# Kernel tuning notes

Hardware: AMD Instinct MI355X
Metric: run time of the kernel (lower is better)

The kernel has to match this reference:

```python
import jax, jax.numpy as jnp
import numpy as np

B, N, C = 2, 2048, 768
H = 16
D = C // H  # head_dim = 48
SCALE = 1.0 / float(np.sqrt(D))


def setup_inputs() -> dict:
    key = jax.random.key(0)
    ks = jax.random.split(key, 5)
    x = jax.random.normal(ks[0], (B, N, C), dtype=jnp.float32)
    # torch nn.Linear weights are [out, in]; apply as x @ W.T
    qkv_w = jax.random.normal(ks[1], (3 * C, C), dtype=jnp.float32) * 0.02
    qkv_b = jax.random.normal(ks[2], (3 * C,), dtype=jnp.float32) * 0.02
    proj_w = jax.random.normal(ks[3], (C, C), dtype=jnp.float32) * 0.02
    proj_b = jax.random.normal(ks[4], (C,), dtype=jnp.float32) * 0.02
    return {"x": x, "qkv_w": qkv_w, "qkv_b": qkv_b, "proj_w": proj_w, "proj_b": proj_b}


def reference(x, qkv_w, qkv_b, proj_w, proj_b):
    # qkv: (B, N, 3C) -> (3, B, H, N, D)
    qkv = x @ qkv_w.T + qkv_b
    qkv = qkv.reshape(B, N, 3, H, D).transpose(2, 0, 3, 1, 4)
    q, k, v = qkv[0], qkv[1], qkv[2]
    # manual attention: full (B, H, N, N) score matrix, as in the original
    attn = jnp.einsum('bhqd,bhkd->bhqk', q, k) * SCALE
    attn = jax.nn.softmax(attn, axis=-1)
    # attn_drop with p=0.0 (eval / deterministic) is identity
    y = jnp.einsum('bhqk,bhkd->bhqd', attn, v)
    y = y.transpose(0, 2, 1, 3).reshape(B, N, C)
    return y @ proj_w.T + proj_b
```

## Files before the change

kernel.cpp:

```cpp
#include <hip/hip_runtime.h>

typedef short v8s __attribute__((ext_vector_type(8)));
typedef short v4s __attribute__((ext_vector_type(4)));
typedef float v4f __attribute__((ext_vector_type(4)));
typedef unsigned uint2v __attribute__((ext_vector_type(2)));
typedef unsigned uint4v __attribute__((ext_vector_type(4)));
typedef unsigned short u16;

#define NSEQ 2048
#define CDIM 768
#define NH   16
#define DH   48
#define DP   64
#define MROWS 4096
#define N3C  2304
#define BH   32

#if __has_builtin(__builtin_amdgcn_exp2f)
#define EXP2(x) __builtin_amdgcn_exp2f(x)
#else
#define EXP2(x) exp2f(x)
#endif
#if __has_builtin(__builtin_amdgcn_rcpf)
#define RCP(x) __builtin_amdgcn_rcpf(x)
#else
#define RCP(x) (1.0f/(x))
#endif

#if __has_builtin(__builtin_amdgcn_permlane32_swap) && __has_builtin(__builtin_amdgcn_permlane16_swap)
#define HAVE_PERMSWAP 1
#endif

__device__ __forceinline__ u16 f2bf(float f){
  unsigned u = __float_as_uint(f);
  u += 0x7FFFu + ((u>>16)&1u);
  return (u16)(u>>16);
}

#if __has_builtin(__builtin_amdgcn_cvt_pk_bf16_f32)
typedef __bf16 bf16x2_t __attribute__((ext_vector_type(2)));
__device__ __forceinline__ unsigned pkbf(float a, float b){
  bf16x2_t r = __builtin_amdgcn_cvt_pk_bf16_f32(a, b);
  return __builtin_bit_cast(unsigned, r);
}
#else
__device__ __forceinline__ unsigned pkbf(float a, float b){
  unsigned x = __float_as_uint(a), y = __float_as_uint(b);
  x += 0x7FFFu + ((x>>16)&1u);
  y += 0x7FFFu + ((y>>16)&1u);
  return (x>>16) | (y & 0xFFFF0000u);
}
#endif

__device__ __forceinline__ void load_lds16(const u16* g, u16* l){
  __builtin_amdgcn_global_load_lds((const __attribute__((address_space(1))) void*)g,
                                   (__attribute__((address_space(3))) void*)l, 16, 0, 0);
}

#define XN8  (MROWS*CDIM/8)
#define WN8  (N3C*CDIM/8)
#define PN8  (CDIM*CDIM/8)
#define CONVB ((XN8+WN8+PN8)/256)
__global__ __launch_bounds__(256) void prep(const float* __restrict__ x, const float* __restrict__ w,
                                            const float* __restrict__ pw, u16* __restrict__ dst,
                                            u16* __restrict__ q, u16* __restrict__ k){
  int bid = blockIdx.x;
  if (bid < CONVB){
    int i = bid*256 + threadIdx.x;
    const float* src;
    if (i < XN8)            src = x  + (size_t)i*8;
    else if (i < XN8+WN8)   src = w  + (size_t)(i - XN8)*8;
    else                    src = pw + (size_t)(i - XN8 - WN8)*8;
    v4f f0 = ((const v4f*)src)[0];
    v4f f1 = ((const v4f*)src)[1];
    v8s o;
#pragma unroll
    for (int j = 0; j < 4; j++) ((u16*)&o)[j]   = f2bf(f0[j]);
#pragma unroll
    for (int j = 0; j < 4; j++) ((u16*)&o)[4+j] = f2bf(f1[j]);
    ((v8s*)dst)[i] = o;
  } else {
    int idx = (bid - CONVB)*256 + threadIdx.x;
    v8s z = (v8s){0,0,0,0,0,0,0,0};
    int r = idx >> 1, half = idx & 1;
    *(v8s*)(q + (size_t)r*DP + DH + half*8) = z;
    *(v8s*)(k + (size_t)r*DP + DH + half*8) = z;
  }
}

__global__ __launch_bounds__(256) void qkv_gemm(const u16* __restrict__ x, const u16* __restrict__ w,
                                                const float* __restrict__ bias,
                                                u16* __restrict__ q, u16* __restrict__ k, u16* __restrict__ v){
  __shared__ __align__(16) u16 As[128*32];
  __shared__ __align__(16) u16 Bs[128*32];
  const int wave = threadIdx.x >> 6;
  const int lane = threadIdx.x & 63;
  const int l15  = lane & 15;
  const int quad = lane >> 4;
  const int wm = wave & 1, wn = wave >> 1;
  const int m0 = blockIdx.x*128, n0 = blockIdx.y*128;

  const int srow = lane >> 2;
  const int sg   = (lane & 3) ^ ((lane >> 3) & 3);
  const int sgoff = sg*8;

  v4f acc[4][4];
#pragma unroll
  for (int i = 0; i < 4; i++)
#pragma unroll
    for (int j = 0; j < 4; j++) acc[i][j] = (v4f){0.f,0.f,0.f,0.f};

  const int sig = (l15 >> 1) & 3;

  for (int kt = 0; kt < CDIM/32; kt++){
    const int k0 = kt*32;
    __syncthreads();
#pragma unroll
    for (int j = 0; j < 2; j++){
      int c = wave*2 + j;
      int r = c*16 + srow;
      load_lds16(x + (size_t)(m0 + r)*CDIM + k0 + sgoff, &As[c*512]);
      load_lds16(w + (size_t)(n0 + r)*CDIM + k0 + sgoff, &Bs[c*512]);
    }
    __syncthreads();

    v8s af[4], bf[4];
#pragma unroll
    for (int t = 0; t < 4; t++){
      int ra = wm*64 + t*16 + l15;
      af[t] = *(const v8s*)(&As[ra*32 + ((quad ^ sig)<<3)]);
      int rb = wn*64 + t*16 + l15;
      bf[t] = *(const v8s*)(&Bs[rb*32 + ((quad ^ sig)<<3)]);
    }
#pragma unroll
    for (int ti = 0; ti < 4; ti++)
#pragma unroll
      for (int tj = 0; tj < 4; tj++)
        acc[ti][tj] = __builtin_amdgcn_mfma_f32_16x16x32_bf16(af[ti], bf[tj], acc[ti][tj], 0, 0, 0);
  }

  const float QS = 0.2082540589f;
#pragma unroll
  for (int tj = 0; tj < 4; tj++){
    const int c = n0 + wn*64 + tj*16 + l15;
    const float bv = bias[c];
    const int t = c / CDIM;
    const int rem = c - t*CDIM;
    const int h = rem / DH;
    const int d = rem - h*DH;
#pragma unroll
    for (int ti = 0; ti < 4; ti++){
#pragma unroll
      for (int r = 0; r < 4; r++){
        int m = m0 + wm*64 + ti*16 + quad*4 + r;
        int b_ = m >> 11;
        int n  = m & (NSEQ-1);
        float val = acc[ti][tj][r] + bv;
        if (t == 0) val *= QS;
        u16 o  = f2bf(val);
        int bhn = b_*NH + h;
        if (t == 0)      q[((size_t)bhn*NSEQ + n)*DP + d] = o;
        else if (t == 1) k[((size_t)bhn*NSEQ + n)*DP + d] = o;
        else             v[((size_t)bhn*DP + d)*NSEQ + n] = o;
      }
    }
  }
}

__global__ __launch_bounds__(256, 4) void attn(const u16* __restrict__ q, const u16* __restrict__ k,
                                               const u16* __restrict__ v, u16* __restrict__ y){
  __shared__ __align__(16) u16 Kl[2][64*64];
  __shared__ __align__(16) u16 Vl[2][48*64];
#ifndef HAVE_PERMSWAP
  __shared__ __align__(16) u16 Pl[4*2*1024];
#endif
  const int bh = blockIdx.x;
  const int qt = blockIdx.y;
  const int wave = threadIdx.x >> 6;
  const int lane = threadIdx.x & 63;
  const int l15  = lane & 15;
  const int quad = lane >> 4;
  const int lo3  = l15 & 7;
  const u16* qb = q + (size_t)bh*NSEQ*DP;
  const u16* kb = k + (size_t)bh*NSEQ*DP;
  const u16* vb = v + (size_t)bh*DP*NSEQ;
  const int qm = qt*128 + wave*32;

  v8s qf[2][2];
#pragma unroll
  for (int si = 0; si < 2; si++)
#pragma unroll
    for (int ks = 0; ks < 2; ks++)
      qf[si][ks] = *(const v8s*)(qb + (size_t)(qm + si*16 + l15)*DP + ks*32 + quad*8);

  const short one = (short)0x3F80;
  const v8s vones = (l15 == 0) ? (v8s){one,one,one,one,one,one,one,one}
                               : (v8s){0,0,0,0,0,0,0,0};

  v4f o[2][4];
#pragma unroll
  for (int si = 0; si < 2; si++)
#pragma unroll
    for (int i = 0; i < 4; i++) o[si][i] = (v4f){0.f,0.f,0.f,0.f};

  const int sr  = lane >> 3;
  const int soff = ((lane & 7) ^ (sr & 7)) * 8;
#ifndef HAVE_PERMSWAP
  u16* Plw = Pl + wave*2048;
#endif

  const int krow0 = wave*8 + sr;
#define STAGE(kt_, b_) do{                                                              \
    load_lds16(kb + ((size_t)((kt_)*64 + krow0))*DP + soff,      &Kl[b_][krow0*64]);    \
    load_lds16(kb + ((size_t)((kt_)*64 + 32 + krow0))*DP + soff, &Kl[b_][(32+krow0)*64]);\
    load_lds16(vb + (size_t)krow0*NSEQ + (kt_)*64 + soff,        &Vl[b_][krow0*64]);    \
    if (wave < 2)                                                                       \
      load_lds16(vb + (size_t)(32+krow0)*NSEQ + (kt_)*64 + soff, &Vl[b_][(32+krow0)*64]);\
  } while(0)

  STAGE(0, 0);

  for (int i = 0; i < 32; i++){
    const int buf = i & 1;
    __syncthreads();
    if (i < 31) STAGE(i + 1, buf^1);

    const u16* Klb = &Kl[buf][0];
    const u16* Vlb = &Vl[buf][0];

    v4f s[2][4];
#pragma unroll
    for (int nt = 0; nt < 4; nt++){
      int rrow = nt*16 + l15;
      v8s kf0 = *(const v8s*)(&Klb[rrow*64 + ((quad ^ lo3)<<3)]);
      v8s kf1 = *(const v8s*)(&Klb[rrow*64 + (((4+quad) ^ lo3)<<3)]);
      s[0][nt] = __builtin_amdgcn_mfma_f32_16x16x32_bf16(kf0, qf[0][0], (v4f){0.f,0.f,0.f,0.f}, 0, 0, 0);
      s[0][nt] = __builtin_amdgcn_mfma_f32_16x16x32_bf16(kf1, qf[0][1], s[0][nt], 0, 0, 0);
      s[1][nt] = __builtin_amdgcn_mfma_f32_16x16x32_bf16(kf0, qf[1][0], (v4f){0.f,0.f,0.f,0.f}, 0, 0, 0);
      s[1][nt] = __builtin_amdgcn_mfma_f32_16x16x32_bf16(kf1, qf[1][1], s[1][nt], 0, 0, 0);
    }

    v8s pa[2][2];
#ifdef HAVE_PERMSWAP
#pragma unroll
    for (int si = 0; si < 2; si++){
      unsigned w[4][2];
#pragma unroll
      for (int nt = 0; nt < 4; nt++){
        w[nt][0] = pkbf(EXP2(s[si][nt][0]), EXP2(s[si][nt][1]));
        w[nt][1] = pkbf(EXP2(s[si][nt][2]), EXP2(s[si][nt][3]));
      }
#pragma unroll
      for (int ks = 0; ks < 2; ks++){
        unsigned W[4];
#pragma unroll
        for (int h = 0; h < 2; h++){
          auto a = __builtin_amdgcn_permlane32_swap(w[2*ks][h], w[2*ks+1][h], false, false);
          auto b = __builtin_amdgcn_permlane16_swap(a[0], a[1], false, false);
          W[h]   = b[0];
          W[2+h] = b[1];
        }
        uint4v u; u[0] = W[0]; u[1] = W[1]; u[2] = W[2]; u[3] = W[3];
        pa[si][ks] = __builtin_bit_cast(v8s, u);
      }
    }
#else
#pragma unroll
    for (int si = 0; si < 2; si++)
#pragma unroll
      for (int nt = 0; nt < 4; nt++){
        uint2v pw;
        pw.x = pkbf(EXP2(s[si][nt][0]), EXP2(s[si][nt][1]));
        pw.y = pkbf(EXP2(s[si][nt][2]), EXP2(s[si][nt][3]));
        int g = nt*2 + (quad>>1);
        *(uint2v*)(&Plw[si*1024 + l15*64 + ((g ^ lo3)<<3) + (quad&1)*4]) = pw;
      }
    __syncthreads();
#pragma unroll
    for (int si = 0; si < 2; si++)
#pragma unroll
      for (int ks = 0; ks < 2; ks++){
        int ga = ks*4 + quad;
        pa[si][ks] = *(const v8s*)(&Plw[si*1024 + l15*64 + ((ga ^ lo3)<<3)]);
      }
#endif

#pragma unroll
    for (int dt = 0; dt < 3; dt++){
#pragma unroll
      for (int ks = 0; ks < 2; ks++){
        int row = dt*16 + l15;
        v8s vf = *(const v8s*)(&Vlb[row*64 + (((ks*4+quad) ^ lo3)<<3)]);
        o[0][dt] = __builtin_amdgcn_mfma_f32_16x16x32_bf16(pa[0][ks], vf, o[0][dt], 0, 0, 0);
        o[1][dt] = __builtin_amdgcn_mfma_f32_16x16x32_bf16(pa[1][ks], vf, o[1][dt], 0, 0, 0);
      }
    }
#pragma unroll
    for (int ks = 0; ks < 2; ks++){
      o[0][3] = __builtin_amdgcn_mfma_f32_16x16x32_bf16(pa[0][ks], vones, o[0][3], 0, 0, 0);
      o[1][3] = __builtin_amdgcn_mfma_f32_16x16x32_bf16(pa[1][ks], vones, o[1][3], 0, 0, 0);
    }
  }

  const int b_ = bh / NH, h = bh % NH;
#pragma unroll
  for (int si = 0; si < 2; si++){
#pragma unroll
    for (int r = 0; r < 4; r++){
      float l = __shfl(o[si][3][r], (lane & 48));
      float inv = RCP(l);
      int rowg = b_*NSEQ + qm + si*16 + quad*4 + r;
#pragma unroll
      for (int dt = 0; dt < 3; dt++)
        y[(size_t)rowg*CDIM + h*DH + dt*16 + l15] = f2bf(o[si][dt][r]*inv);
    }
  }
#undef STAGE
}

__global__ __launch_bounds__(256) void proj_gemm(const u16* __restrict__ y, const u16* __restrict__ w,
                                                 const float* __restrict__ bias, float* __restrict__ out){
  __shared__ __align__(16) u16 As[64*32];
  __shared__ __align__(16) u16 Bs[64*32];
  const int wave = threadIdx.x >> 6;
  const int lane = threadIdx.x & 63;
  const int l15  = lane & 15;
  const int quad = lane >> 4;
  const int wm = wave & 1, wn = wave >> 1;
  const int m0 = blockIdx.x*64, n0 = blockIdx.y*64;

  const int srow = lane >> 2;
  const int sg   = (lane & 3) ^ ((lane >> 3) & 3);
  const int sgoff = sg*8;

  v4f acc[2][2];
#pragma unroll
  for (int i = 0; i < 2; i++)
#pragma unroll
    for (int j = 0; j < 2; j++) acc[i][j] = (v4f){0.f,0.f,0.f,0.f};

  const int sig = (l15 >> 1) & 3;
  const int rS = wave*16 + srow;

  for (int kt = 0; kt < CDIM/32; kt++){
    const int k0 = kt*32;
    __syncthreads();
    load_lds16(y + (size_t)(m0 + rS)*CDIM + k0 + sgoff, &As[wave*512]);
    load_lds16(w + (size_t)(n0 + rS)*CDIM + k0 + sgoff, &Bs[wave*512]);
    __syncthreads();

    v8s af[2], bf[2];
#pragma unroll
    for (int t = 0; t < 2; t++){
      int ra = wm*32 + t*16 + l15;
      af[t] = *(const v8s*)(&As[ra*32 + ((quad ^ sig)<<3)]);
      int rb = wn*32 + t*16 + l15;
      bf[t] = *(const v8s*)(&Bs[rb*32 + ((quad ^ sig)<<3)]);
    }
#pragma unroll
    for (int ti = 0; ti < 2; ti++)
#pragma unroll
      for (int tj = 0; tj < 2; tj++)
        acc[ti][tj] = __builtin_amdgcn_mfma_f32_16x16x32_bf16(af[ti], bf[tj], acc[ti][tj], 0, 0, 0);
  }

#pragma unroll
  for (int tj = 0; tj < 2; tj++){
    const int c = n0 + wn*32 + tj*16 + l15;
    const float bv = bias[c];
#pragma unroll
    for (int ti = 0; ti < 2; ti++){
#pragma unroll
      for (int r = 0; r < 4; r++){
        int m = m0 + wm*32 + ti*16 + quad*4 + r;
        out[(size_t)m*CDIM + c] = acc[ti][tj][r] + bv;
      }
    }
  }
}

extern "C" void kernel_launch(void* const* d_in, const int* in_sizes, int n_in,
                              void* d_out, int out_size, void* d_ws, size_t ws_size,
                              hipStream_t stream){
  const float* x      = (const float*)d_in[0];
  const float* qkv_w  = (const float*)d_in[1];
  const float* qkv_b  = (const float*)d_in[2];
  const float* proj_w = (const float*)d_in[3];
  const float* proj_b = (const float*)d_in[4];
  float* out = (float*)d_out;

  u16* xb  = (u16*)d_ws;
  u16* wb  = xb  + (size_t)MROWS*CDIM;
  u16* pwb = wb  + (size_t)N3C*CDIM;
  u16* q   = pwb + (size_t)CDIM*CDIM;
  u16* k   = q + (size_t)BH*NSEQ*DP;
  u16* v   = k + (size_t)BH*NSEQ*DP;
  u16* y = xb;

  prep<<<dim3(CONVB + 512), dim3(256), 0, stream>>>(x, qkv_w, proj_w, xb, q, k);
  qkv_gemm<<<dim3(MROWS/128, N3C/128), dim3(256), 0, stream>>>(xb, wb, qkv_b, q, k, v);
  attn<<<dim3(BH, NSEQ/128), dim3(256), 0, stream>>>(q, k, v, y);
  proj_gemm<<<dim3(MROWS/64, CDIM/64), dim3(256), 0, stream>>>(y, pwb, proj_b, out);
}
```

Measured before the change: 163.8 us.

## Load K/V fragments straight to registers and remap blocks per XCD

The attention kernel no longer stages K and V tiles through double-buffered shared memory. Each wave now loads its MFMA fragments for K and V directly from global memory into registers, using a two-tile register ping-pong that prefetches the next tile while the current one computes. This removes the per-iteration block barrier and the LDS traffic. Blocks are also launched on a 1D grid and remapped so that all query tiles of a head land on the same XCD, improving L2 reuse of K/V. In exchange, each wave re-reads K/V from cache (four times the global/L2 traffic), register pressure rises, and the occupancy hint drops to 2.

```diff
diff --git a/kernel.cpp b/kernel.cpp
--- a/kernel.cpp
+++ b/kernel.cpp
@@ -167,20 +167,19 @@
   }
 }
 
-__global__ __launch_bounds__(256, 4) void attn(const u16* __restrict__ q, const u16* __restrict__ k,
+__global__ __launch_bounds__(256, 2) void attn(const u16* __restrict__ q, const u16* __restrict__ k,
                                                const u16* __restrict__ v, u16* __restrict__ y){
-  __shared__ __align__(16) u16 Kl[2][64*64];
-  __shared__ __align__(16) u16 Vl[2][48*64];
 #ifndef HAVE_PERMSWAP
   __shared__ __align__(16) u16 Pl[4*2*1024];
 #endif
-  const int bh = blockIdx.x;
-  const int qt = blockIdx.y;
+  const int lin = blockIdx.x;
+  const int xcd = lin & 7, jj = lin >> 3;
+  const int bh  = xcd*4 + (jj >> 4);
+  const int qt  = jj & 15;
   const int wave = threadIdx.x >> 6;
   const int lane = threadIdx.x & 63;
   const int l15  = lane & 15;
   const int quad = lane >> 4;
-  const int lo3  = l15 & 7;
   const u16* qb = q + (size_t)bh*NSEQ*DP;
   const u16* kb = k + (size_t)bh*NSEQ*DP;
   const u16* vb = v + (size_t)bh*DP*NSEQ;
@@ -203,103 +202,110 @@
 #pragma unroll
     for (int i = 0; i < 4; i++) o[si][i] = (v4f){0.f,0.f,0.f,0.f};
 
-  const int sr  = lane >> 3;
-  const int soff = ((lane & 7) ^ (sr & 7)) * 8;
+  const u16* kfb = kb + (size_t)l15*DP + quad*8;
+  const u16* vfb = vb + (size_t)l15*NSEQ + quad*8;
+
 #ifndef HAVE_PERMSWAP
   u16* Plw = Pl + wave*2048;
 #endif
 
-  const int krow0 = wave*8 + sr;
-#define STAGE(kt_, b_) do{                                                              \
-    load_lds16(kb + ((size_t)((kt_)*64 + krow0))*DP + soff,      &Kl[b_][krow0*64]);    \
-    load_lds16(kb + ((size_t)((kt_)*64 + 32 + krow0))*DP + soff, &Kl[b_][(32+krow0)*64]);\
-    load_lds16(vb + (size_t)krow0*NSEQ + (kt_)*64 + soff,        &Vl[b_][krow0*64]);    \
-    if (wave < 2)                                                                       \
-      load_lds16(vb + (size_t)(32+krow0)*NSEQ + (kt_)*64 + soff, &Vl[b_][(32+krow0)*64]);\
+#define LOADT(t_, K0_, K1_, VF_) do{                                                    \
+    _Pragma("unroll")                                                                   \
+    for (int nt = 0; nt < 4; nt++){                                                     \
+      const u16* kp = kfb + (size_t)((t_)*64 + nt*16)*DP;                               \
+      K0_[nt] = *(const v8s*)(kp);                                                      \
+      K1_[nt] = *(const v8s*)(kp + 32);                                                 \
+    }                                                                                   \
+    _Pragma("unroll")                                                                   \
+    for (int dt = 0; dt < 3; dt++)                                                      \
+      _Pragma("unroll")                                                                 \
+      for (int ks = 0; ks < 2; ks++)                                                    \
+        VF_[dt*2+ks] = *(const v8s*)(vfb + (size_t)dt*16*NSEQ + (t_)*64 + ks*32);       \
   } while(0)
 
-  STAGE(0, 0);
-
-  for (int i = 0; i < 32; i++){
-    const int buf = i & 1;
-    __syncthreads();
-    if (i < 31) STAGE(i + 1, buf^1);
-
-    const u16* Klb = &Kl[buf][0];
-    const u16* Vlb = &Vl[buf][0];
-
-    v4f s[2][4];
-#pragma unroll
-    for (int nt = 0; nt < 4; nt++){
-      int rrow = nt*16 + l15;
-      v8s kf0 = *(const v8s*)(&Klb[rrow*64 + ((quad ^ lo3)<<3)]);
-      v8s kf1 = *(const v8s*)(&Klb[rrow*64 + (((4+quad) ^ lo3)<<3)]);
-      s[0][nt] = __builtin_amdgcn_mfma_f32_16x16x32_bf16(kf0, qf[0][0], (v4f){0.f,0.f,0.f,0.f}, 0, 0, 0);
-      s[0][nt] = __builtin_amdgcn_mfma_f32_16x16x32_bf16(kf1, qf[0][1], s[0][nt], 0, 0, 0);
-      s[1][nt] = __builtin_amdgcn_mfma_f32_16x16x32_bf16(kf0, qf[1][0], (v4f){0.f,0.f,0.f,0.f}, 0, 0, 0);
-      s[1][nt] = __builtin_amdgcn_mfma_f32_16x16x32_bf16(kf1, qf[1][1], s[1][nt], 0, 0, 0);
-    }
-
-    v8s pa[2][2];
 #ifdef HAVE_PERMSWAP
-#pragma unroll
-    for (int si = 0; si < 2; si++){
-      unsigned w[4][2];
-#pragma unroll
-      for (int nt = 0; nt < 4; nt++){
-        w[nt][0] = pkbf(EXP2(s[si][nt][0]), EXP2(s[si][nt][1]));
-        w[nt][1] = pkbf(EXP2(s[si][nt][2]), EXP2(s[si][nt][3]));
+#define PTRANS                                                                          \
+    _Pragma("unroll")                                                                   \
+    for (int si = 0; si < 2; si++){                                                     \
+      unsigned w[4][2];                                                                 \
+      _Pragma("unroll")                                                                 \
+      for (int nt = 0; nt < 4; nt++){                                                   \
+        w[nt][0] = pkbf(EXP2(s[si][nt][0]), EXP2(s[si][nt][1]));                        \
+        w[nt][1] = pkbf(EXP2(s[si][nt][2]), EXP2(s[si][nt][3]));                        \
+      }                                                                                 \
+      _Pragma("unroll")                                                                 \
+      for (int ks = 0; ks < 2; ks++){                                                   \
+        unsigned W[4];                                                                  \
+        _Pragma("unroll")                                                               \
+        for (int h = 0; h < 2; h++){                                                    \
+          auto a = __builtin_amdgcn_permlane32_swap(w[2*ks][h], w[2*ks+1][h], false, false); \
+          auto b = __builtin_amdgcn_permlane16_swap(a[0], a[1], false, false);          \
+          W[h]   = b[0];                                                                \
+          W[2+h] = b[1];                                                                \
+        }                                                                               \
+        uint4v u; u[0] = W[0]; u[1] = W[1]; u[2] = W[2]; u[3] = W[3];                   \
+        pa[si][ks] = __builtin_bit_cast(v8s, u);                                        \
+      }                                                                                 \
+    }
+#else
+#define PTRANS                                                                          \
+    _Pragma("unroll")                                                                   \
+    for (int si = 0; si < 2; si++)                                                      \
+      _Pragma("unroll")                                                                 \
+      for (int nt = 0; nt < 4; nt++){                                                   \
+        uint2v pw;                                                                      \
+        pw.x = pkbf(EXP2(s[si][nt][0]), EXP2(s[si][nt][1]));                            \
+        pw.y = pkbf(EXP2(s[si][nt][2]), EXP2(s[si][nt][3]));                            \
+        int lo3 = l15 & 7;                                                              \
+        int g = nt*2 + (quad>>1);                                                       \
+        *(uint2v*)(&Plw[si*1024 + l15*64 + ((g ^ lo3)<<3) + (quad&1)*4]) = pw;          \
+      }                                                                                 \
+    __syncthreads();                                                                    \
+    _Pragma("unroll")                                                                   \
+    for (int si = 0; si < 2; si++)                                                      \
+      _Pragma("unroll")                                                                 \
+      for (int ks = 0; ks < 2; ks++){                                                   \
+        int lo3 = l15 & 7;                                                              \
+        int ga = ks*4 + quad;                                                           \
+        pa[si][ks] = *(const v8s*)(&Plw[si*1024 + l15*64 + ((ga ^ lo3)<<3)]);           \
       }
-#pragma unroll
-      for (int ks = 0; ks < 2; ks++){
-        unsigned W[4];
-#pragma unroll
-        for (int h = 0; h < 2; h++){
-          auto a = __builtin_amdgcn_permlane32_swap(w[2*ks][h], w[2*ks+1][h], false, false);
-          auto b = __builtin_amdgcn_permlane16_swap(a[0], a[1], false, false);
-          W[h]   = b[0];
-          W[2+h] = b[1];
-        }
-        uint4v u; u[0] = W[0]; u[1] = W[1]; u[2] = W[2]; u[3] = W[3];
-        pa[si][ks] = __builtin_bit_cast(v8s, u);
-      }
-    }
-#else
-#pragma unroll
-    for (int si = 0; si < 2; si++)
-#pragma unroll
-      for (int nt = 0; nt < 4; nt++){
-        uint2v pw;
-        pw.x = pkbf(EXP2(s[si][nt][0]), EXP2(s[si][nt][1]));
-        pw.y = pkbf(EXP2(s[si][nt][2]), EXP2(s[si][nt][3]));
-        int g = nt*2 + (quad>>1);
-        *(uint2v*)(&Plw[si*1024 + l15*64 + ((g ^ lo3)<<3) + (quad&1)*4]) = pw;
-      }
-    __syncthreads();
-#pragma unroll
-    for (int si = 0; si < 2; si++)
-#pragma unroll
-      for (int ks = 0; ks < 2; ks++){
-        int ga = ks*4 + quad;
-        pa[si][ks] = *(const v8s*)(&Plw[si*1024 + l15*64 + ((ga ^ lo3)<<3)]);
-      }
-#endif
-
-#pragma unroll
-    for (int dt = 0; dt < 3; dt++){
-#pragma unroll
-      for (int ks = 0; ks < 2; ks++){
-        int row = dt*16 + l15;
-        v8s vf = *(const v8s*)(&Vlb[row*64 + (((ks*4+quad) ^ lo3)<<3)]);
-        o[0][dt] = __builtin_amdgcn_mfma_f32_16x16x32_bf16(pa[0][ks], vf, o[0][dt], 0, 0, 0);
-        o[1][dt] = __builtin_amdgcn_mfma_f32_16x16x32_bf16(pa[1][ks], vf, o[1][dt], 0, 0, 0);
-      }
-    }
-#pragma unroll
-    for (int ks = 0; ks < 2; ks++){
-      o[0][3] = __builtin_amdgcn_mfma_f32_16x16x32_bf16(pa[0][ks], vones, o[0][3], 0, 0, 0);
-      o[1][3] = __builtin_amdgcn_mfma_f32_16x16x32_bf16(pa[1][ks], vones, o[1][3], 0, 0, 0);
-    }
+#endif
+
+#define COMPUTE(K0_, K1_, VF_) do{                                                      \
+    v4f s[2][4];                                                                        \
+    _Pragma("unroll")                                                                   \
+    for (int nt = 0; nt < 4; nt++){                                                     \
+      s[0][nt] = __builtin_amdgcn_mfma_f32_16x16x32_bf16(K0_[nt], qf[0][0], (v4f){0.f,0.f,0.f,0.f}, 0, 0, 0); \
+      s[0][nt] = __builtin_amdgcn_mfma_f32_16x16x32_bf16(K1_[nt], qf[0][1], s[0][nt], 0, 0, 0); \
+      s[1][nt] = __builtin_amdgcn_mfma_f32_16x16x32_bf16(K0_[nt], qf[1][0], (v4f){0.f,0.f,0.f,0.f}, 0, 0, 0); \
+      s[1][nt] = __builtin_amdgcn_mfma_f32_16x16x32_bf16(K1_[nt], qf[1][1], s[1][nt], 0, 0, 0); \
+    }                                                                                   \
+    v8s pa[2][2];                                                                       \
+    PTRANS                                                                              \
+    _Pragma("unroll")                                                                   \
+    for (int dt = 0; dt < 3; dt++){                                                     \
+      _Pragma("unroll")                                                                 \
+      for (int ks = 0; ks < 2; ks++){                                                   \
+        o[0][dt] = __builtin_amdgcn_mfma_f32_16x16x32_bf16(pa[0][ks], VF_[dt*2+ks], o[0][dt], 0, 0, 0); \
+        o[1][dt] = __builtin_amdgcn_mfma_f32_16x16x32_bf16(pa[1][ks], VF_[dt*2+ks], o[1][dt], 0, 0, 0); \
+      }                                                                                 \
+    }                                                                                   \
+    _Pragma("unroll")                                                                   \
+    for (int ks = 0; ks < 2; ks++){                                                     \
+      o[0][3] = __builtin_amdgcn_mfma_f32_16x16x32_bf16(pa[0][ks], vones, o[0][3], 0, 0, 0); \
+      o[1][3] = __builtin_amdgcn_mfma_f32_16x16x32_bf16(pa[1][ks], vones, o[1][3], 0, 0, 0); \
+    }                                                                                   \
+  } while(0)
+
+  v8s k0A[4], k1A[4], vfA[6];
+  v8s k0B[4], k1B[4], vfB[6];
+
+  LOADT(0, k0A, k1A, vfA);
+  for (int t = 0; t < 32; t += 2){
+    LOADT(t + 1, k0B, k1B, vfB);
+    COMPUTE(k0A, k1A, vfA);
+    if (t + 2 < 32) LOADT(t + 2, k0A, k1A, vfA);
+    COMPUTE(k0B, k1B, vfB);
   }
 
   const int b_ = bh / NH, h = bh % NH;
@@ -315,7 +321,9 @@
         y[(size_t)rowg*CDIM + h*DH + dt*16 + l15] = f2bf(o[si][dt][r]*inv);
     }
   }
-#undef STAGE
+#undef LOADT
+#undef COMPUTE
+#undef PTRANS
 }
 
 __global__ __launch_bounds__(256) void proj_gemm(const u16* __restrict__ y, const u16* __restrict__ w,
@@ -399,6 +407,6 @@
 
   prep<<<dim3(CONVB + 512), dim3(256), 0, stream>>>(x, qkv_w, proj_w, xb, q, k);
   qkv_gemm<<<dim3(MROWS/128, N3C/128), dim3(256), 0, stream>>>(xb, wb, qkv_b, q, k, v);
-  attn<<<dim3(BH, NSEQ/128), dim3(256), 0, stream>>>(q, k, v, y);
+  attn<<<dim3(BH*NSEQ/128), dim3(256), 0, stream>>>(q, k, v, y);
   proj_gemm<<<dim3(MROWS/64, CDIM/64), dim3(256), 0, stream>>>(y, pwb, proj_b, out);
 }
```

After: 221.1 us. +35.0%, slower.
